# Optimization experiments

Hardware: AMD Instinct MI355X
Metric: run time of the kernel (lower is better)

## Reference

```python
import jax, jax.numpy as jnp
import numpy as np

D_IN = 1024
D_OUT = 1024
NUM_HEADS = 16
HEAD_DIM = D_OUT // NUM_HEADS


def setup_inputs() -> dict:
    key = jax.random.key(0)
    k1, k2, k3, k4 = jax.random.split(key, 4)
    x = jax.random.normal(k1, (2, 2048, D_IN), dtype=jnp.float32)
    # Linear weights stored torch-style [out_features, in_features]
    W_qkv = jax.random.normal(k2, (3 * D_OUT, D_IN), dtype=jnp.float32) * (1.0 / np.sqrt(D_IN))
    W_out = jax.random.normal(k3, (D_OUT, D_OUT), dtype=jnp.float32) * (1.0 / np.sqrt(D_OUT))
    b_out = jax.random.normal(k4, (D_OUT,), dtype=jnp.float32) * 0.01
    return {"x": x, "W_qkv": W_qkv, "W_out": W_out, "b_out": b_out}


def reference(x, W_qkv, W_out, b_out):
    b, s, _ = x.shape
    qkv = jnp.einsum('bsi,oi->bso', x, W_qkv)  # [b, s, 3*d_out]
    q, k, v = jnp.split(qkv, 3, axis=-1)
    def to_heads(t):
        return t.reshape(b, s, NUM_HEADS, HEAD_DIM).transpose(0, 2, 1, 3)
    q, k, v = to_heads(q), to_heads(k), to_heads(v)
    # NOTE: original module does NOT scale by 1/sqrt(head_dim)
    scores = jnp.einsum('bhqd,bhkd->bhqk', q, k)
    causal = jnp.tril(jnp.ones((s, s), dtype=bool))  # True = keep
    scores = jnp.where(causal[None, None], scores, -jnp.inf)
    attn = jax.nn.softmax(scores, axis=-1)
    ctx = jnp.einsum('bhqk,bhkd->bhqd', attn, v)
    ctx = ctx.transpose(0, 2, 1, 3).reshape(b, s, D_OUT)
    return jnp.einsum('bso,po->bsp', ctx, W_out) + b_out
```

## Files before the change

### kernel.cpp

```cpp
#include <hip/hip_runtime.h>
#include <cstdint>
#include <cstddef>


typedef __attribute__((ext_vector_type(8))) short bf16x8;
typedef __attribute__((ext_vector_type(4))) float f32x4;

#define LOG2E 1.44269504f

#define MFMA16(a, b, c) __builtin_amdgcn_mfma_f32_16x16x32_bf16((a), (b), (c), 0, 0, 0)

#define GLDS16(g, s)                                                        \
  __builtin_amdgcn_global_load_lds(                                         \
      (const __attribute__((address_space(1))) void*)(g),                   \
      (__attribute__((address_space(3))) void*)(s), 16, 0, 0)

#define ASYNC_BAR(N) asm volatile("s_waitcnt vmcnt(" #N ")\n\ts_barrier" ::: "memory")

#if __has_builtin(__builtin_amdgcn_exp2f)
#define EXP2F(x) __builtin_amdgcn_exp2f(x)
#else
#define EXP2F(x) exp2f(x)
#endif

static __device__ __forceinline__ unsigned short f2bf(float f) {
  unsigned int u = __builtin_bit_cast(unsigned int, f);
  u += 0x7FFFu + ((u >> 16) & 1u);
  return (unsigned short)(u >> 16);
}

static __device__ __forceinline__ unsigned int pk2bf(float a, float b) {
  const unsigned int ua = __builtin_bit_cast(unsigned int, a) + 0x8000u;
  const unsigned int ub = __builtin_bit_cast(unsigned int, b) + 0x8000u;
  return __builtin_amdgcn_perm(ub, ua, 0x07060302);
}

__global__ __launch_bounds__(256) void cast_bf16(const float* __restrict__ x,
                                                 const float* __restrict__ wq,
                                                 const float* __restrict__ wo,
                                                 unsigned short* __restrict__ xb,
                                                 unsigned short* __restrict__ wqb,
                                                 unsigned short* __restrict__ wob)
{
  const int id = blockIdx.x * 256 + threadIdx.x;
  const float* src;
  unsigned short* dst;
  int off;
  if (id < 1048576)               { src = x;  dst = xb;  off = id; }
  else if (id < 1048576 + 786432) { src = wq; dst = wqb; off = id - 1048576; }
  else                            { src = wo; dst = wob; off = id - (1048576 + 786432); }
  float4 v = ((const float4*)src)[off];
  ushort4 o;
  o.x = f2bf(v.x); o.y = f2bf(v.y); o.z = f2bf(v.z); o.w = f2bf(v.w);
  ((ushort4*)dst)[off] = o;
}

template <int MODE>
__global__ __launch_bounds__(256) void gemm_bt(const unsigned short* __restrict__ A,
                                               const unsigned short* __restrict__ B,
                                               const float* __restrict__ bias,
                                               float* __restrict__ OutF,
                                               unsigned short* __restrict__ Qb,
                                               unsigned short* __restrict__ Kb,
                                               unsigned short* __restrict__ Vt)
{
  __shared__ unsigned short pool[24576];

  const int tid  = threadIdx.x;
  const int wave = tid >> 6, lane = tid & 63, quad = lane >> 4, cl = lane & 15;
  const int wm = wave >> 1, wn = wave & 1;
  const int m0 = blockIdx.y * 128, n0 = blockIdx.x * 128;
  const int sr = lane >> 2, sc = lane & 3;

  const int part = (MODE == 1) ? (n0 >> 10) : 0;
  const bool swapped = (MODE == 0) || (part < 2);

  f32x4 acc[4][4];
  #pragma unroll
  for (int i = 0; i < 4; ++i)
    #pragma unroll
    for (int j = 0; j < 4; ++j)
      #pragma unroll
      for (int r = 0; r < 4; ++r) acc[i][j][r] = 0.f;

  const int scs = (sc ^ ((sr >> 1) & 3)) * 8;
  const int rchunk = (quad ^ ((cl >> 1) & 3)) * 8;

  auto stage = [&](int k0, int buf) {
    unsigned short* As = pool + buf * 8192;
    unsigned short* Bs = As + 4096;
    #pragma unroll
    for (int ii = 0; ii < 2; ++ii) {
      const int r = wave * 32 + ii * 16 + sr;
      GLDS16(A + (size_t)(m0 + r) * 1024 + k0 + scs, &As[(wave * 32 + ii * 16) * 32]);
      GLDS16(B + (size_t)(n0 + r) * 1024 + k0 + scs, &Bs[(wave * 32 + ii * 16) * 32]);
    }
  };

  stage(0, 0);
  stage(32, 1);
  int cur = 0;
  #pragma unroll 1
  for (int it = 0; it < 32; ++it) {
    if (it + 2 < 32) {
      ASYNC_BAR(4);
      const int bnx = (cur == 0) ? 2 : cur - 1;
      stage((it + 2) * 32, bnx);
    } else if (it + 1 < 32) {
      ASYNC_BAR(4);
    } else {
      ASYNC_BAR(0);
    }

    const unsigned short* As = pool + cur * 8192;
    const unsigned short* Bs = As + 4096;
    bf16x8 af[4], bfr[4];
    #pragma unroll
    for (int mt = 0; mt < 4; ++mt)
      af[mt] = *(const bf16x8*)&As[(wm * 64 + mt * 16 + cl) * 32 + rchunk];
    #pragma unroll
    for (int nt = 0; nt < 4; ++nt)
      bfr[nt] = *(const bf16x8*)&Bs[(wn * 64 + nt * 16 + cl) * 32 + rchunk];

    if (swapped) {
      #pragma unroll
      for (int mt = 0; mt < 4; ++mt)
        #pragma unroll
        for (int nt = 0; nt < 4; ++nt)
          acc[mt][nt] = MFMA16(bfr[nt], af[mt], acc[mt][nt]);
    } else {
      #pragma unroll
      for (int mt = 0; mt < 4; ++mt)
        #pragma unroll
        for (int nt = 0; nt < 4; ++nt)
          acc[mt][nt] = MFMA16(af[mt], bfr[nt], acc[mt][nt]);
    }
    cur = (cur == 2) ? 0 : cur + 1;
  }

  if (MODE == 1) {
    const int bb = m0 >> 11, ss = m0 & 2047;
    if (part == 2) {
      #pragma unroll
      for (int half = 0; half < 2; ++half) {
        __syncthreads();
        if (wn == half) {
          #pragma unroll
          for (int mt = 0; mt < 4; ++mt)
            #pragma unroll
            for (int nt = 0; nt < 4; ++nt) {
              const int nl = nt * 16 + cl;
              const int ml = wm * 64 + mt * 16 + quad * 4;
              ushort4 pk;
              pk.x = f2bf(acc[mt][nt][0]); pk.y = f2bf(acc[mt][nt][1]);
              pk.z = f2bf(acc[mt][nt][2]); pk.w = f2bf(acc[mt][nt][3]);
              *(ushort4*)&pool[nl * 136 + ml] = pk;
            }
        }
        __syncthreads();
        const int row = tid >> 2, q4 = tid & 3;
        const int nglob = n0 + half * 64 + row;
        const int hh = (nglob >> 6) & 15, d = nglob & 63;
        unsigned short* drow = Vt + ((size_t)(bb * 16 + hh) * 64 + d) * 2048 + ss;
        #pragma unroll
        for (int i = 0; i < 4; ++i) {
          const bf16x8 v = *(const bf16x8*)&pool[row * 136 + q4 * 32 + i * 8];
          *(bf16x8*)(drow + q4 * 32 + i * 8) = v;
        }
      }
    } else {
      unsigned short* dst = (part == 0) ? Qb : Kb;
      const float sc2 = (part == 0) ? LOG2E : 1.0f;
      #pragma unroll
      for (int mt = 0; mt < 4; ++mt) {
        const int m = ss + wm * 64 + mt * 16 + cl;
        #pragma unroll
        for (int nt = 0; nt < 4; ++nt) {
          const int np = (n0 & 1023) + wn * 64 + nt * 16 + quad * 4;
          const int hh = np >> 6, d0 = np & 63;
          ushort4 pk;
          pk.x = f2bf(acc[mt][nt][0] * sc2);
          pk.y = f2bf(acc[mt][nt][1] * sc2);
          pk.z = f2bf(acc[mt][nt][2] * sc2);
          pk.w = f2bf(acc[mt][nt][3] * sc2);
          *(ushort4*)&dst[((size_t)(bb * 16 + hh) * 2048 + m) * 64 + d0] = pk;
        }
      }
    }
  } else {
    #pragma unroll
    for (int mt = 0; mt < 4; ++mt) {
      const int m = m0 + wm * 64 + mt * 16 + cl;
      #pragma unroll
      for (int nt = 0; nt < 4; ++nt) {
        const int n = n0 + wn * 64 + nt * 16 + quad * 4;
        const float4 bv = *(const float4*)(bias + n);
        float4 o;
        o.x = acc[mt][nt][0] + bv.x; o.y = acc[mt][nt][1] + bv.y;
        o.z = acc[mt][nt][2] + bv.z; o.w = acc[mt][nt][3] + bv.w;
        *(float4*)&OutF[(size_t)m * 1024 + n] = o;
      }
    }
  }
}

__global__ __launch_bounds__(256) void attn_mfma(const unsigned short* __restrict__ Qb,
                                                 const unsigned short* __restrict__ Kb,
                                                 const unsigned short* __restrict__ Vt,
                                                 unsigned short* __restrict__ CTX)
{
  __shared__ unsigned short Ksm[3][64 * 64];
  __shared__ unsigned short Vsm[3][64 * 64];
  __shared__ unsigned short Psm[4][32 * 40];

  const int tid  = threadIdx.x;
  const int wave = tid >> 6, lane = tid & 63, quad = lane >> 4, cl = lane & 15;

  const int L  = blockIdx.x;
  const int bh = 4 * (L & 7) + ((L >> 3) & 3);
  const int b  = bh >> 4, h = bh & 15;
  const int p  = L >> 5;
  const int g  = p * 4 + wave;
  const int qlo = g * 16;
  const int qhi = (127 - g) * 16;
  const size_t base = (size_t)bh * (2048 * 64);

  bf16x8 qf[2][2];
  #pragma unroll
  for (int dk = 0; dk < 2; ++dk) {
    qf[0][dk] = *(const bf16x8*)(Qb + base + (size_t)(qlo + cl) * 64 + dk * 32 + quad * 8);
    qf[1][dk] = *(const bf16x8*)(Qb + base + (size_t)(qhi + cl) * 64 + dk * 32 + quad * 8);
  }

  f32x4 oacc[2][4];
  #pragma unroll
  for (int mf = 0; mf < 2; ++mf)
    #pragma unroll
    for (int dt = 0; dt < 4; ++dt)
      #pragma unroll
      for (int r = 0; r < 4; ++r) oacc[mf][dt][r] = 0.f;
  float lr[2][4] = {};

  bf16x8 ones;
  #pragma unroll
  for (int k = 0; k < 8; ++k) ones[k] = (short)0x3F80;

  const int lrow  = lane >> 3;
  const int lslot = (lane & 7) ^ lrow;
  const int nch = 32 - p;

  auto stageKV = [&](int j64, int buf) {
    #pragma unroll
    for (int ii = 0; ii < 2; ++ii) {
      const int r0 = wave * 16 + ii * 8;
      GLDS16(Kb + base + (size_t)(j64 + r0 + lrow) * 64 + lslot * 8, &Ksm[buf][r0 * 64]);
      GLDS16(Vt + base + (size_t)(r0 + lrow) * 2048 + j64 + lslot * 8, &Vsm[buf][r0 * 64]);
    }
  };

  stageKV(0, 0);
  stageKV(64, 1);
  int cur = 0;
  #pragma unroll 1
  for (int ch = 0; ch < nch; ++ch) {
    if (ch + 2 < nch) {
      ASYNC_BAR(4);
      const int bnx = (cur == 0) ? 2 : cur - 1;
      stageKV((ch + 2) * 64, bnx);
    } else if (ch + 1 < nch) {
      ASYNC_BAR(4);
    } else {
      ASYNC_BAR(0);
    }

    const int j64 = ch * 64;
    #pragma unroll
    for (int jli = 0; jli < 2; ++jli) {
      const int jg0 = j64 + jli * 32;
      if (jg0 > qhi + 15) continue;
      const bool lowAct = (jg0 <= qlo + 15);
      const int jl = jli * 32;

      bf16x8 kf[2][2];
      #pragma unroll
      for (int jf = 0; jf < 2; ++jf)
        #pragma unroll
        for (int dk = 0; dk < 2; ++dk) {
          const int jrow = jl + jf * 16 + cl;
          const int slot = (dk * 4 + quad) ^ (cl & 7);
          kf[jf][dk] = *(const bf16x8*)&Ksm[cur][jrow * 64 + slot * 8];
        }

      f32x4 st[2][2];
      #pragma unroll
      for (int jf = 0; jf < 2; ++jf)
        #pragma unroll
        for (int mf = 0; mf < 2; ++mf) {
          if (mf == 0 && !lowAct) continue;
          f32x4 z;
          #pragma unroll
          for (int r = 0; r < 4; ++r) z[r] = 0.f;
          z = MFMA16(kf[jf][0], qf[mf][0], z);
          st[jf][mf] = MFMA16(kf[jf][1], qf[mf][1], z);
        }

      #pragma unroll
      for (int mf = 0; mf < 2; ++mf) {
        if (mf == 0 && !lowAct) continue;
        const int qbase = mf ? qhi : qlo;
        const bool diag = (jg0 + 32 > qbase);
        #pragma unroll
        for (int jf = 0; jf < 2; ++jf) {
          float pv[4];
          if (diag) {
            const int qg = qbase + cl;
            #pragma unroll
            for (int r = 0; r < 4; ++r) {
              const int jg = jg0 + jf * 16 + quad * 4 + r;
              pv[r] = (jg <= qg) ? EXP2F(st[jf][mf][r]) : 0.f;
            }
          } else {
            #pragma unroll
            for (int r = 0; r < 4; ++r) pv[r] = EXP2F(st[jf][mf][r]);
          }
          uint2 w;
          w.x = pk2bf(pv[0], pv[1]);
          w.y = pk2bf(pv[2], pv[3]);
          *(uint2*)&Psm[wave][(mf * 16 + cl) * 40 + jf * 16 + quad * 4] = w;
        }
      }

      bf16x8 vf[4];
      #pragma unroll
      for (int dt = 0; dt < 4; ++dt) {
        const int d = dt * 16 + cl;
        const int slot = ((jl >> 3) + quad) ^ (cl & 7);
        vf[dt] = *(const bf16x8*)&Vsm[cur][d * 64 + slot * 8];
      }

      #pragma unroll
      for (int mf = 0; mf < 2; ++mf) {
        if (mf == 0 && !lowAct) continue;
        const bf16x8 pf = *(const bf16x8*)&Psm[wave][(mf * 16 + cl) * 40 + quad * 8];
        f32x4 z;
        #pragma unroll
        for (int r = 0; r < 4; ++r) z[r] = 0.f;
        const f32x4 ls = MFMA16(pf, ones, z);
        #pragma unroll
        for (int r = 0; r < 4; ++r) lr[mf][r] += ls[r];
        #pragma unroll
        for (int dt = 0; dt < 4; ++dt)
          oacc[mf][dt] = MFMA16(pf, vf[dt], oacc[mf][dt]);
      }
    }
    cur = (cur == 2) ? 0 : cur + 1;
  }

  #pragma unroll
  for (int mf = 0; mf < 2; ++mf) {
    const int qbase = mf ? qhi : qlo;
    float inv[4];
    #pragma unroll
    for (int r = 0; r < 4; ++r) inv[r] = 1.f / lr[mf][r];
    #pragma unroll
    for (int dt = 0; dt < 4; ++dt)
      #pragma unroll
      for (int r = 0; r < 4; ++r)
        CTX[(size_t)(b * 2048 + qbase + quad * 4 + r) * 1024 +
            h * 64 + dt * 16 + cl] = f2bf(oacc[mf][dt][r] * inv[r]);
  }
}

extern "C" void kernel_launch(void* const* d_in, const int* in_sizes, int n_in,
                              void* d_out, int out_size, void* d_ws, size_t ws_size,
                              hipStream_t stream)
{
  const float* x    = (const float*)d_in[0];
  const float* Wqkv = (const float*)d_in[1];
  const float* Wout = (const float*)d_in[2];
  const float* bout = (const float*)d_in[3];
  float* out = (float*)d_out;

  char* ws = (char*)d_ws;
  unsigned short* xb  = (unsigned short*)(ws);
  unsigned short* wqb = (unsigned short*)(ws + 8388608);
  unsigned short* wob = (unsigned short*)(ws + 14680064);
  unsigned short* Qb  = (unsigned short*)(ws + 16777216);
  unsigned short* Kb  = (unsigned short*)(ws + 25165824);
  unsigned short* Vt  = (unsigned short*)(ws + 33554432);
  unsigned short* CTX = (unsigned short*)(ws + 41943040);

  cast_bf16<<<dim3(8192), dim3(256), 0, stream>>>(x, Wqkv, Wout, xb, wqb, wob);

  gemm_bt<1><<<dim3(24, 32), dim3(256), 0, stream>>>(xb, wqb, nullptr, nullptr, Qb, Kb, Vt);

  attn_mfma<<<dim3(512), dim3(256), 0, stream>>>(Qb, Kb, Vt, CTX);

  gemm_bt<0><<<dim3(8, 32), dim3(256), 0, stream>>>(CTX, wob, bout, out, nullptr, nullptr, nullptr);
}
```

Before: 196.5 us.

## Add dedicated 256x256-tile QKV GEMM with XCD-aware block mapping

Replaces the generic 128x128 QKV projection GEMM with a new kernel that uses 512 threads, 256x256 output tiles, double-buffered async global-to-LDS loads with swizzled layout, and interleaved staging between MFMA sub-blocks. Blocks are remapped so neighbouring tiles land on the same XCD for L2 reuse, and the MFMA operand order is swapped for Q/K to simplify the epilogue. The larger tiles cut redundant global loads, but the grid of 192 blocks is small relative to the CU count and the heavy register and LDS use limits occupancy.

```diff
diff --git a/kernel.cpp b/kernel.cpp
--- a/kernel.cpp
+++ b/kernel.cpp
@@ -16,6 +16,7 @@
       (__attribute__((address_space(3))) void*)(s), 16, 0, 0)
 
 #define ASYNC_BAR(N) asm volatile("s_waitcnt vmcnt(" #N ")\n\ts_barrier" ::: "memory")
+#define BAR() asm volatile("s_barrier" ::: "memory")
 
 #if __has_builtin(__builtin_amdgcn_exp2f)
 #define EXP2F(x) __builtin_amdgcn_exp2f(x)
@@ -55,6 +56,185 @@
   ((ushort4*)dst)[off] = o;
 }
 
+#define MMAC(AF, BF, MS, NS)                                                       \
+  do {                                                                             \
+    __builtin_amdgcn_s_setprio(1);                                                 \
+    if (swapped) {                                                                 \
+      _Pragma("unroll")                                                            \
+      for (int mt = 0; mt < 4; ++mt)                                               \
+        _Pragma("unroll")                                                          \
+        for (int nt = 0; nt < 2; ++nt) {                                           \
+          acc[(MS)*4+mt][(NS)*2+nt] = MFMA16(BF[nt][0], AF[mt][0], acc[(MS)*4+mt][(NS)*2+nt]); \
+          acc[(MS)*4+mt][(NS)*2+nt] = MFMA16(BF[nt][1], AF[mt][1], acc[(MS)*4+mt][(NS)*2+nt]); \
+        }                                                                          \
+    } else {                                                                       \
+      _Pragma("unroll")                                                            \
+      for (int mt = 0; mt < 4; ++mt)                                               \
+        _Pragma("unroll")                                                          \
+        for (int nt = 0; nt < 2; ++nt) {                                           \
+          acc[(MS)*4+mt][(NS)*2+nt] = MFMA16(AF[mt][0], BF[nt][0], acc[(MS)*4+mt][(NS)*2+nt]); \
+          acc[(MS)*4+mt][(NS)*2+nt] = MFMA16(AF[mt][1], BF[nt][1], acc[(MS)*4+mt][(NS)*2+nt]); \
+        }                                                                          \
+    }                                                                              \
+    __builtin_amdgcn_s_setprio(0);                                                 \
+  } while (0)
+
+__global__ __launch_bounds__(512, 2) void gemm_qkv(const unsigned short* __restrict__ A,
+                                                   const unsigned short* __restrict__ B,
+                                                   unsigned short* __restrict__ Qb,
+                                                   unsigned short* __restrict__ Kb,
+                                                   unsigned short* __restrict__ Vt)
+{
+  __shared__ unsigned short pool[65536];
+
+  const int tid  = threadIdx.x;
+  const int wave = tid >> 6, lane = tid & 63, quad = lane >> 4, cl = lane & 15;
+  const int wm = wave >> 2, wn = wave & 3;
+
+  const int bid = blockIdx.x;
+  const int xcd = bid & 7, j = bid >> 3;
+  const int mb = (xcd >> 1) * 4 + j / 6;
+  const int nb = (xcd & 1) * 6 + j % 6;
+  const int m0 = mb * 256, n0 = nb * 256;
+  const int part = nb >> 2;
+  const bool swapped = (part < 2);
+
+  const int lrow = lane >> 3;
+  const int sg   = (lane & 7) ^ (((lane >> 5) & 1) << 1);
+
+  auto stageA = [&](int h0, int buf, int k0) {
+    #pragma unroll
+    for (int ii = 0; ii < 2; ++ii) {
+      const int r0 = h0 + wave * 16 + ii * 8;
+      GLDS16(A + (size_t)(m0 + r0 + lrow) * 1024 + k0 + sg * 8,
+             &pool[buf * 32768 + r0 * 64]);
+    }
+  };
+  auto stageB = [&](int h0, int buf, int k0) {
+    #pragma unroll
+    for (int ii = 0; ii < 2; ++ii) {
+      const int r0 = h0 + wave * 16 + ii * 8;
+      GLDS16(B + (size_t)(n0 + r0 + lrow) * 1024 + k0 + sg * 8,
+             &pool[buf * 32768 + 16384 + r0 * 64]);
+    }
+  };
+
+  const int rswz = ((cl >> 2) & 1) << 1;
+  auto loadA = [&](bf16x8 (&af)[4][2], int msub, int b) {
+    const unsigned short* base = &pool[b * 32768];
+    #pragma unroll
+    for (int mt = 0; mt < 4; ++mt) {
+      const int row = wm * 128 + msub * 64 + mt * 16 + cl;
+      #pragma unroll
+      for (int kk = 0; kk < 2; ++kk)
+        af[mt][kk] = *(const bf16x8*)&base[row * 64 + ((kk * 4 + quad) ^ rswz) * 8];
+    }
+  };
+  auto loadB = [&](bf16x8 (&bf)[2][2], int nsub, int b) {
+    const unsigned short* base = &pool[b * 32768 + 16384];
+    #pragma unroll
+    for (int nt = 0; nt < 2; ++nt) {
+      const int row = wn * 64 + nsub * 32 + nt * 16 + cl;
+      #pragma unroll
+      for (int kk = 0; kk < 2; ++kk)
+        bf[nt][kk] = *(const bf16x8*)&base[row * 64 + ((kk * 4 + quad) ^ rswz) * 8];
+    }
+  };
+
+  f32x4 acc[8][4];
+  #pragma unroll
+  for (int i = 0; i < 8; ++i)
+    #pragma unroll
+    for (int jj = 0; jj < 4; ++jj)
+      #pragma unroll
+      for (int r = 0; r < 4; ++r) acc[i][jj][r] = 0.f;
+
+  stageB(0,   0, 0);
+  stageA(0,   0, 0);
+  stageB(128, 0, 0);
+  stageA(128, 0, 0);
+  stageB(0,   1, 64);
+  stageA(0,   1, 64);
+
+  #pragma unroll 1
+  for (int t = 0; t < 16; ++t) {
+    const int b = t & 1, bn = b ^ 1;
+    const int kc  = (t + 1) * 64;
+    const int kc2 = (t + 2) * 64;
+
+    bf16x8 af[4][2], bfA[2][2], bfB[2][2];
+
+    if (t < 15) { ASYNC_BAR(4); } else { ASYNC_BAR(0); }
+    loadA(af, 0, b);
+    loadB(bfA, 0, b);
+    if (t < 15) stageB(128, bn, kc);
+    MMAC(af, bfA, 0, 0);
+
+    loadB(bfB, 1, b);
+    if (t < 15) stageA(128, bn, kc);
+    MMAC(af, bfB, 0, 1);
+
+    BAR();
+    loadA(af, 1, b);
+    if (t < 14) stageB(0, b, kc2);
+    MMAC(af, bfB, 1, 1);
+
+    BAR();
+    if (t < 14) stageA(0, b, kc2);
+    MMAC(af, bfA, 1, 0);
+  }
+
+  const int bb = m0 >> 11, ss = m0 & 2047;
+  if (part < 2) {
+    unsigned short* dst = (part == 0) ? Qb : Kb;
+    const float sc2 = (part == 0) ? LOG2E : 1.0f;
+    const int npb = (n0 & 1023) + wn * 64;
+    #pragma unroll
+    for (int mt = 0; mt < 8; ++mt) {
+      const int m = ss + wm * 128 + mt * 16 + cl;
+      #pragma unroll
+      for (int nt = 0; nt < 4; ++nt) {
+        const int np = npb + nt * 16 + quad * 4;
+        const int hh = np >> 6, d0 = np & 63;
+        ushort4 pk;
+        pk.x = f2bf(acc[mt][nt][0] * sc2);
+        pk.y = f2bf(acc[mt][nt][1] * sc2);
+        pk.z = f2bf(acc[mt][nt][2] * sc2);
+        pk.w = f2bf(acc[mt][nt][3] * sc2);
+        *(ushort4*)&dst[((size_t)(bb * 16 + hh) * 2048 + m) * 64 + d0] = pk;
+      }
+    }
+  } else {
+    unsigned short* trans = pool;
+    #pragma unroll 1
+    for (int r = 0; r < 2; ++r) {
+      __syncthreads();
+      if ((wn >> 1) == r) {
+        #pragma unroll
+        for (int mt = 0; mt < 8; ++mt) {
+          const int s_l = wm * 128 + mt * 16 + quad * 4;
+          #pragma unroll
+          for (int nt = 0; nt < 4; ++nt) {
+            const int n_l = (wn & 1) * 64 + nt * 16 + cl;
+            ushort4 pk;
+            pk.x = f2bf(acc[mt][nt][0]); pk.y = f2bf(acc[mt][nt][1]);
+            pk.z = f2bf(acc[mt][nt][2]); pk.w = f2bf(acc[mt][nt][3]);
+            *(ushort4*)&trans[n_l * 264 + s_l] = pk;
+          }
+        }
+      }
+      __syncthreads();
+      const int row = tid >> 2, q4 = tid & 3;
+      const int nv = (n0 & 1023) + r * 128 + row;
+      const int hh = nv >> 6, d = nv & 63;
+      unsigned short* drow = Vt + ((size_t)(bb * 16 + hh) * 64 + d) * 2048 + ss + q4 * 64;
+      #pragma unroll
+      for (int i = 0; i < 8; ++i)
+        *(bf16x8*)(drow + i * 8) = *(const bf16x8*)&trans[row * 264 + q4 * 64 + i * 8];
+    }
+  }
+}
+
 template <int MODE>
 __global__ __launch_bounds__(256) void gemm_bt(const unsigned short* __restrict__ A,
                                                const unsigned short* __restrict__ B,
@@ -392,7 +572,7 @@
 
   cast_bf16<<<dim3(8192), dim3(256), 0, stream>>>(x, Wqkv, Wout, xb, wqb, wob);
 
-  gemm_bt<1><<<dim3(24, 32), dim3(256), 0, stream>>>(xb, wqb, nullptr, nullptr, Qb, Kb, Vt);
+  gemm_qkv<<<dim3(192), dim3(512), 0, stream>>>(xb, wqb, Qb, Kb, Vt);
 
   attn_mfma<<<dim3(512), dim3(256), 0, stream>>>(Qb, Kb, Vt, CTX);
 
```

Measured after the change: 189.7 us. -3.5%, faster.
